# Optimization experiments

Hardware: AMD Instinct MI355X
Metric: run time of the kernel (lower is better)

## Reference

```python
import jax, jax.numpy as jnp
import numpy as np

M1 = M2 = 16      # spectral modes
CM1 = CM2 = 4     # cft modes = modes // 4
L_SEG = 4
M_CHEB = 8
PAD = 9


def _cft2d(x):
    # x: [B,C,H,W]; H,W divisible by L_SEG, segment length divisible by M_CHEB
    B, C, H, W = x.shape
    hs, ws = H // L_SEG, W // L_SEG
    seg = x.reshape(B, C, L_SEG, hs, L_SEG, ws).transpose(0, 1, 2, 4, 3, 5)
    seg = seg.reshape(B, C, L_SEG * L_SEG, hs * ws)  # row-major segment order (i,j)
    seg = seg / jnp.maximum(jnp.linalg.norm(seg, axis=-1, keepdims=True), 1e-12)
    # torch x[:,:,k::M].mean over k=0..M-1 == reshape (n//M, M), mean over rows
    coeffs = seg.reshape(B, C, L_SEG * L_SEG, (hs * ws) // M_CHEB, M_CHEB).mean(axis=3)
    coeffs = coeffs.reshape(B, C, -1)[:, :, : CM1 * CM2]
    return coeffs.reshape(B, C, CM1, CM2)  # real part; imag part is zero


def _spectral_rc(x, w1, w2, g1w, g1b, g2w, g2b):
    B, C, H, W = x.shape
    xft = jnp.fft.rfft2(x, axes=(-2, -1))
    top = jnp.einsum('bixy,ioxy->boxy', xft[:, :, :M1, :M2], w1)
    bot = jnp.einsum('bixy,ioxy->boxy', xft[:, :, H - M1:, :M2], w2)
    out_ft = jnp.zeros((B, w1.shape[1], H, W // 2 + 1), dtype=xft.dtype)
    out_ft = out_ft.at[:, :, :M1, :M2].set(top)
    out_ft = out_ft.at[:, :, H - M1:, :M2].set(bot)
    x_fno = jnp.fft.irfft2(out_ft, s=(H, W), axes=(-2, -1))
    cr = _cft2d(x)
    # torch.view_as_real interleaves (real, imag) on last axis; imag == 0
    cflat = jnp.stack([cr, jnp.zeros_like(cr)], axis=-1).reshape(B, -1)
    h = jax.nn.gelu(cflat @ g1w.T + g1b, approximate=False)
    corr = h @ g2w.T + g2b  # [B, C_out]
    return x_fno + corr[:, :, None, None]


def _forward(x, sw1r, sw1i, sw2r, sw2i, g1w, g1b, g2w, g2b, cw, cb,
             fc0w, fc0b, fc1w, fc1b, fc2w, fc2b):
    B, S1, S2, _ = x.shape
    gx = jnp.broadcast_to(jnp.linspace(0., 1., S1, dtype=x.dtype)[None, :, None, None], (B, S1, S2, 1))
    gy = jnp.broadcast_to(jnp.linspace(0., 1., S2, dtype=x.dtype)[None, None, :, None], (B, S1, S2, 1))
    h = jnp.concatenate([x, gx, gy], axis=-1) @ fc0w.T + fc0b
    h = h.transpose(0, 3, 1, 2)
    h = jnp.pad(h, ((0, 0), (0, 0), (0, PAD), (0, PAD)))
    for l in range(4):
        w1 = sw1r[l] + 1j * sw1i[l]
        w2 = sw2r[l] + 1j * sw2i[l]
        h1 = _spectral_rc(h, w1, w2, g1w[l], g1b[l], g2w[l], g2b[l])
        h2 = jnp.einsum('bchw,oc->bohw', h, cw[l]) + cb[l][None, :, None, None]
        h = h1 + h2
        if l < 3:
            h = jax.nn.gelu(h, approximate=False)
    h = h[..., :-PAD, :-PAD].transpose(0, 2, 3, 1)
    h = jax.nn.gelu(h @ fc1w.T + fc1b, approximate=False)
    return h @ fc2w.T + fc2b


def setup_inputs():
    key = jax.random.key(0)
    ks = jax.random.split(key, 20)
    B, S, Cin, Cout, Wd = 8, 119, 3, 1, 64
    f32 = jnp.float32
    scale = 1.0 / (Wd * Wd)
    return {
        'x': jax.random.normal(ks[0], (B, S, S, Cin), f32),
        'sw1r': scale * jax.random.uniform(ks[1], (4, Wd, Wd, M1, M2), f32),
        'sw1i': scale * jax.random.uniform(ks[2], (4, Wd, Wd, M1, M2), f32),
        'sw2r': scale * jax.random.uniform(ks[3], (4, Wd, Wd, M1, M2), f32),
        'sw2i': scale * jax.random.uniform(ks[4], (4, Wd, Wd, M1, M2), f32),
        'g1w': 0.02 * jax.random.normal(ks[5], (4, 256, 2048), f32),
        'g1b': 0.02 * jax.random.normal(ks[6], (4, 256), f32),
        'g2w': 0.02 * jax.random.normal(ks[7], (4, Wd, 256), f32),
        'g2b': 0.02 * jax.random.normal(ks[8], (4, Wd), f32),
        'cw': (1.0 / 8.0) * jax.random.normal(ks[9], (4, Wd, Wd), f32),
        'cb': 0.1 * jax.random.normal(ks[10], (4, Wd), f32),
        'fc0w': 0.4 * jax.random.normal(ks[11], (Wd, Cin + 2), f32),
        'fc0b': 0.1 * jax.random.normal(ks[12], (Wd,), f32),
        'fc1w': (1.0 / 8.0) * jax.random.normal(ks[13], (128, Wd), f32),
        'fc1b': 0.1 * jax.random.normal(ks[14], (128,), f32),
        'fc2w': (1.0 / 11.3) * jax.random.normal(ks[15], (Cout, 128), f32),
        'fc2b': 0.1 * jax.random.normal(ks[16], (Cout,), f32),
    }


def reference(x, sw1r, sw1i, sw2r, sw2i, g1w, g1b, g2w, g2b, cw, cb,
              fc0w, fc0b, fc1w, fc1b, fc2w, fc2b):
    return _forward(x, sw1r, sw1i, sw2r, sw2i, g1w, g1b, g2w, g2b, cw, cb,
                    fc0w, fc0b, fc1w, fc1b, fc2w, fc2b)
```

## Files before the change

### kernel.cpp

```cpp
#include <hip/hip_runtime.h>
#include <math.h>

#define NB 8
#define NC 64
#define NH 128
#define NW 128
#define NS 119
#define NPIX 113288

typedef __attribute__((ext_vector_type(8))) short bf16x8;
typedef __attribute__((ext_vector_type(4))) float f32x4;
typedef __attribute__((ext_vector_type(4))) unsigned short ushort4v;

__device__ __forceinline__ float gelu_f(float v) {
    return 0.5f * v * (1.0f + erff(v * 0.70710678118654752f));
}

__device__ __forceinline__ unsigned short f2bf(float x) {
    unsigned int u = __builtin_bit_cast(unsigned int, x);
    u += 0x7FFFu + ((u >> 16) & 1u);
    return (unsigned short)(u >> 16);
}

__global__ void __launch_bounds__(128) k_trig(float2* __restrict__ trig) {
    int t = threadIdx.x;
    double a = (double)t * (3.14159265358979323846 / 64.0);
    trig[t] = make_float2((float)cos(a), (float)sin(a));
}

__global__ void __launch_bounds__(256) k_tabm(short* __restrict__ wmf) {
    int idx = blockIdx.x * 256 + threadIdx.x;
    int f = idx >> 9;
    int l = (idx >> 3) & 63;
    int e = idx & 7;
    int ni = f >> 2, k = f & 3;
    int w = k * 32 + (l >> 4) * 8 + e;
    int n = ni * 16 + (l & 15);
    int q = n >> 1;
    int prod = (q * w) & 127;
    double a = (double)prod * (3.14159265358979323846 / 64.0);
    float v = (float)((n & 1) ? -sin(a) : cos(a));
    wmf[idx] = (short)f2bf(v);
}

__global__ void __launch_bounds__(256) k_tc(const float* __restrict__ fc1w,
                                            const float* __restrict__ cw,
                                            float* __restrict__ fc1wT,
                                            float* __restrict__ cwT) {
    int u = blockIdx.x * 256 + threadIdx.x;
    if (u < 8192) {
        int c = u >> 7, j = u & 127;
        fc1wT[u] = fc1w[j * 64 + c];
    } else {
        int v = u - 8192;
        int l = v >> 12, idx = v & 4095;
        int c = idx >> 6, o = idx & 63;
        cwT[v] = cw[l * 4096 + o * 64 + c];
    }
}

__global__ void __launch_bounds__(256) k_fc0(const float* __restrict__ x,
                                             const float* __restrict__ w,
                                             const float* __restrict__ bia,
                                             float* __restrict__ h) {
    __shared__ float sw[320];
    __shared__ float sb[64];
    int t = threadIdx.x;
    for (int u = t; u < 320; u += 256) sw[u] = w[u];
    if (t < 64) sb[t] = bia[t];
    __syncthreads();
    int p = blockIdx.x * 256 + t;
    int b = p >> 14;
    int rem = p & 16383;
    int r = rem >> 7, wc = rem & 127;
    float v0 = 0.f, v1 = 0.f, v2 = 0.f, gx = 0.f, gy = 0.f;
    bool inside = (r < NS) && (wc < NS);
    if (inside) {
        const float* xp = x + ((size_t)(b * NS + r) * NS + wc) * 3;
        v0 = xp[0]; v1 = xp[1]; v2 = xp[2];
        gx = (float)r * (1.0f / 118.0f);
        gy = (float)wc * (1.0f / 118.0f);
    }
    float* hp = h + (size_t)b * NC * NH * NW + rem;
    for (int c = 0; c < 64; ++c) {
        float val = 0.f;
        if (inside) {
            const float* wr = sw + c * 5;
            val = v0 * wr[0] + v1 * wr[1] + v2 * wr[2] + gx * wr[3] + gy * wr[4] + sb[c];
        }
        hp[c * (NH * NW)] = val;
    }
}

__global__ void __launch_bounds__(256) k_dft2(const float* __restrict__ h,
                                              float2* __restrict__ xft,
                                              float* __restrict__ cr,
                                              const short* __restrict__ wmf,
                                              const float2* __restrict__ trig) {
    __shared__ __align__(16) short sxb[32][136];
    __shared__ float2 sT[128][17];
    __shared__ float2 st[128];
    __shared__ float s_cs[2][32][8];
    __shared__ float s_cq[2][32][8];
    int t = threadIdx.x;
    int bc = blockIdx.x;
    if (t < 128) st[t] = trig[t];
    int lane = t & 63, wv = t >> 6;
    int mi = wv >> 1, ni = wv & 1;
    bf16x8 bfrag[4];
    {
        const short* wp = wmf + ((size_t)(ni * 4) * 64 + lane) * 8;
#pragma unroll
        for (int k = 0; k < 4; ++k) bfrag[k] = *(const bf16x8*)(wp + k * 512);
    }
    const float* src = h + (size_t)bc * 16384;
    const short* abase = &sxb[mi * 16 + (lane & 15)][(lane >> 4) * 8];
    for (int it = 0; it < 4; ++it) {
        __syncthreads();
#pragma unroll
        for (int j = 0; j < 4; ++j) {
            int idx4 = t + j * 256;
            float4 v = *(const float4*)(src + (size_t)it * 4096 + (size_t)idx4 * 4);
            ushort4v pk;
            pk.x = f2bf(v.x); pk.y = f2bf(v.y); pk.z = f2bf(v.z); pk.w = f2bf(v.w);
            int row = idx4 >> 5, c4 = (idx4 & 31) * 4;
            *(ushort4v*)(&sxb[row][c4]) = pk;
        }
        if (it == 0) {
            int rr = t >> 3, k = t & 7;
            const float* rowp = src + rr * 128;
            float cs0 = 0.f, cq0 = 0.f, cs1 = 0.f, cq1 = 0.f;
#pragma unroll
            for (int g = 0; g < 4; ++g) {
                float a = rowp[g * 8 + k];       cs0 += a;  cq0 += a * a;
                float b = rowp[32 + g * 8 + k];  cs1 += b;  cq1 += b * b;
            }
            s_cs[0][rr][k] = cs0; s_cs[1][rr][k] = cs1;
            s_cq[0][rr][k] = cq0; s_cq[1][rr][k] = cq1;
        }
        __syncthreads();
        f32x4 D = {0.f, 0.f, 0.f, 0.f};
#pragma unroll
        for (int k = 0; k < 4; ++k) {
            bf16x8 a = *(const bf16x8*)(abase + k * 32);
            D = __builtin_amdgcn_mfma_f32_16x16x32_bf16(a, bfrag[k], D, 0, 0, 0);
        }
        int row = it * 32 + mi * 16 + ((lane >> 4) << 2);
        int col = ni * 16 + (lane & 15);
        float* sTf = (float*)&sT[0][0];
#pragma unroll
        for (int r = 0; r < 4; ++r) sTf[(size_t)(row + r) * 34 + col] = D[r];
    }
    __syncthreads();
    int ky = t & 15;
    int mlo = t >> 4;
    int kxa = mlo, kxb = 112 + mlo;
    float2 sva = st[kxa]; float sca = sva.x, ssa = -sva.y;
    float2 svb = st[kxb]; float scb = svb.x, ssb = -svb.y;
    float rea = 0.f, ima = 0.f, reb = 0.f, imb = 0.f;
    for (int h0 = 0; h0 < 128; h0 += 16) {
        float2 bva = st[(kxa * h0) & 127]; float cca = bva.x, csa = -bva.y;
        float2 bvb = st[(kxb * h0) & 127]; float ccb = bvb.x, csb = -bvb.y;
#pragma unroll
        for (int j = 0; j < 16; ++j) {
            float2 Tv = sT[h0 + j][ky];
            rea += Tv.x * cca - Tv.y * csa;
            ima += Tv.x * csa + Tv.y * cca;
            reb += Tv.x * ccb - Tv.y * csb;
            imb += Tv.x * csb + Tv.y * ccb;
            float na = cca * sca - csa * ssa; csa = cca * ssa + csa * sca; cca = na;
            float nb = ccb * scb - csb * ssb; csb = ccb * ssb + csb * scb; ccb = nb;
        }
    }
    float2* xp = xft + (size_t)bc * 512;
    xp[mlo * 16 + ky] = make_float2(rea, ima);
    xp[(mlo + 16) * 16 + ky] = make_float2(reb, imb);
    if (t < 16) {
        int half = t >> 3, k = t & 7;
        float s = 0.f, q = 0.f;
        for (int rr = 0; rr < 32; ++rr) {
            s += s_cs[half][rr][k];
#pragma unroll
            for (int kk = 0; kk < 8; ++kk) q += s_cq[half][rr][kk];
        }
        float norm = fmaxf(sqrtf(q), 1e-12f);
        cr[bc * 16 + t] = s / (128.0f * norm);
    }
}

__global__ void __launch_bounds__(512) k_mixmlp(const float2* __restrict__ xft,
                                                const float* __restrict__ w1r,
                                                const float* __restrict__ w1i,
                                                const float* __restrict__ w2r,
                                                const float* __restrict__ w2i,
                                                const float* __restrict__ cr,
                                                const float* __restrict__ g1w,
                                                const float* __restrict__ g1b,
                                                float* __restrict__ hmid,
                                                float2* __restrict__ F) {
    __shared__ __align__(16) char smem[36864];
    int t = threadIdx.x;
    int bid = blockIdx.x;
    if (bid < 512) {
        float2* s_w = (float2*)smem;
        float2* s_x = (float2*)(smem + 32768);
        int m = (bid & 7) + 8 * ((bid >> 3) & 3);
        int e = bid >> 5;
        const float* wr; const float* wi; int mm;
        if (m < 16) { wr = w1r; wi = w1i; mm = m; } else { wr = w2r; wi = w2i; mm = m - 16; }
        int off = mm * 16 + e;
        for (int u = t; u < 4096; u += 512) {
            s_w[u] = make_float2(wr[(u << 8) + off], wi[(u << 8) + off]);
        }
        {
            int bb = t >> 6, i = t & 63;
            s_x[bb * 64 + i] = xft[((size_t)(bb * 64 + i) * 32 + m) * 16 + e];
        }
        __syncthreads();
        int bb = t >> 6, o = t & 63;
        float re = 0.f, im = 0.f;
#pragma unroll 8
        for (int i = 0; i < 64; ++i) {
            float2 xv = s_x[bb * 64 + i];
            float2 wv = s_w[i * 64 + o];
            re += xv.x * wv.x - xv.y * wv.y;
            im += xv.x * wv.y + xv.y * wv.x;
        }
        F[((size_t)(bb * 16 + e) * 32 + m) * 64 + o] = make_float2(re, im);
    } else {
        float* s_cr   = (float*)smem;
        float* s_wave = (float*)(smem + 32768);
        int j = bid - 512;
        for (int u = t; u < 8192; u += 512) s_cr[u] = cr[u];
        const float* wrow = g1w + (size_t)j * 2048;
        float w0 = wrow[4 * t], w1 = wrow[4 * t + 2];
        __syncthreads();
        float acc[8];
#pragma unroll
        for (int b = 0; b < 8; ++b) {
            float2 v = *(const float2*)(s_cr + b * 1024 + 2 * t);
            acc[b] = v.x * w0 + v.y * w1;
        }
#pragma unroll
        for (int d = 32; d > 0; d >>= 1) {
#pragma unroll
            for (int b = 0; b < 8; ++b) acc[b] += __shfl_down(acc[b], d, 64);
        }
        int wv = t >> 6;
        if ((t & 63) == 0) {
#pragma unroll
            for (int b = 0; b < 8; ++b) s_wave[wv * 8 + b] = acc[b];
        }
        __syncthreads();
        if (t < 8) {
            float a = g1b[j];
            for (int q = 0; q < 8; ++q) a += s_wave[q * 8 + t];
            hmid[t * 256 + j] = gelu_f(a);
        }
    }
}

__global__ void __launch_bounds__(256, 4) k_invb(const float2* __restrict__ F,
                                                 const float* __restrict__ hin,
                                                 const float* __restrict__ cwTl,
                                                 const float* __restrict__ cbl,
                                                 const float* __restrict__ hmid,
                                                 const float* __restrict__ g2w,
                                                 const float* __restrict__ g2b,
                                                 const float2* __restrict__ trig,
                                                 float* __restrict__ hout,
                                                 int do_gelu) {
    int blk = blockIdx.x;
    int b = blk >> 7, h = blk & 127;
    __shared__ __align__(16) float s_cwT[64][64];
    __shared__ __align__(16) float2 s_g[16][64];
    __shared__ float2 s_t[128];
    __shared__ float s_co[64];
    __shared__ float s_part[4][64];
    int t = threadIdx.x;
    if (t < 128) s_t[t] = trig[t];
    {
        float* cw0 = &s_cwT[0][0];
        for (int u = t; u < 4096; u += 256) cw0[u] = cwTl[u];
    }
    {
        int o = t & 63, q = t >> 6;
        const float* hv = hmid + b * 256 + q * 64;
        const float* gw = g2w + o * 256 + q * 64;
        float a = 0.f;
#pragma unroll 8
        for (int v = 0; v < 64; ++v) a += hv[v] * gw[v];
        s_part[q][o] = a;
    }
    {
        int o = t & 63, ky0 = t >> 6;
        const float2* Fb = F + (size_t)b * 32768 + o;
        float a0r=0.f,a0i=0.f,a1r=0.f,a1i=0.f,a2r=0.f,a2i=0.f,a3r=0.f,a3i=0.f;
#pragma unroll 4
        for (int m = 0; m < 32; ++m) {
            int kx = (m < 16) ? m : (96 + m);
            float2 wz = trig[(kx * h) & 127];
            const float2* fm = Fb + m * 64;
            float2 f0 = fm[(ky0     ) * 2048];
            float2 f1 = fm[(ky0 +  4) * 2048];
            float2 f2 = fm[(ky0 +  8) * 2048];
            float2 f3 = fm[(ky0 + 12) * 2048];
            a0r += f0.x*wz.x - f0.y*wz.y; a0i += f0.x*wz.y + f0.y*wz.x;
            a1r += f1.x*wz.x - f1.y*wz.y; a1i += f1.x*wz.y + f1.y*wz.x;
            a2r += f2.x*wz.x - f2.y*wz.y; a2i += f2.x*wz.y + f2.y*wz.x;
            a3r += f3.x*wz.x - f3.y*wz.y; a3i += f3.x*wz.y + f3.y*wz.x;
        }
        s_g[ky0     ][o] = make_float2(a0r, a0i);
        s_g[ky0 +  4][o] = make_float2(a1r, a1i);
        s_g[ky0 +  8][o] = make_float2(a2r, a2i);
        s_g[ky0 + 12][o] = make_float2(a3r, a3i);
    }
    __syncthreads();
    if (t < 64)
        s_co[t] = s_part[0][t] + s_part[1][t] + s_part[2][t] + s_part[3][t]
                + g2b[t] + cbl[t];
    int ot2 = t >> 6;
    int wt6 = t & 63;
    int o0 = ot2 * 16;
    float acc[16][2];
#pragma unroll
    for (int i = 0; i < 16; ++i) { acc[i][0] = 0.f; acc[i][1] = 0.f; }
    float2 rw0 = s_t[wt6];
    float2 rw1 = s_t[wt6 + 64];
    float z0r = 1.f, z0i = 0.f, z1r = 1.f, z1i = 0.f;
    const float invn = 1.0f / 16384.0f;
    for (int ky = 0; ky < 16; ++ky) {
        float fs = (ky == 0) ? invn : (2.f * invn);
        float tc0 = fs * z0r, ts0 = fs * z0i;
        float tc1 = fs * z1r, ts1 = fs * z1i;
        const float4* gk = (const float4*)(&s_g[ky][o0]);
#pragma unroll
        for (int i2 = 0; i2 < 8; ++i2) {
            float4 g2 = gk[i2];
            acc[2*i2][0]   += g2.x * tc0 - g2.y * ts0;
            acc[2*i2][1]   += g2.x * tc1 - g2.y * ts1;
            acc[2*i2+1][0] += g2.z * tc0 - g2.w * ts0;
            acc[2*i2+1][1] += g2.z * tc1 - g2.w * ts1;
        }
        float nz0 = z0r * rw0.x - z0i * rw0.y; z0i = z0r * rw0.y + z0i * rw0.x; z0r = nz0;
        float nz1 = z1r * rw1.x - z1i * rw1.y; z1i = z1r * rw1.y + z1i * rw1.x; z1r = nz1;
    }
    const float* hp = hin + ((size_t)(b * 64) * 128 + h) * 128;
    for (int cc = 0; cc < 64; cc += 4) {
        float hv0[4], hv1[4];
#pragma unroll
        for (int c = 0; c < 4; ++c) {
            hv0[c] = hp[(size_t)(cc + c) * 16384 + wt6];
            hv1[c] = hp[(size_t)(cc + c) * 16384 + wt6 + 64];
        }
#pragma unroll
        for (int c = 0; c < 4; ++c) {
            const float4* cwp = (const float4*)(&s_cwT[cc + c][o0]);
#pragma unroll
            for (int i4 = 0; i4 < 4; ++i4) {
                float4 cv = cwp[i4];
                acc[4*i4][0]   += cv.x * hv0[c]; acc[4*i4][1]   += cv.x * hv1[c];
                acc[4*i4+1][0] += cv.y * hv0[c]; acc[4*i4+1][1] += cv.y * hv1[c];
                acc[4*i4+2][0] += cv.z * hv0[c]; acc[4*i4+2][1] += cv.z * hv1[c];
                acc[4*i4+3][0] += cv.w * hv0[c]; acc[4*i4+3][1] += cv.w * hv1[c];
            }
        }
    }
    __syncthreads();
#pragma unroll
    for (int i = 0; i < 16; ++i) {
        int o = o0 + i;
        float co = s_co[o];
        float* outp = hout + ((size_t)(b * 64 + o) * 128 + h) * 128;
        float v0 = acc[i][0] + co;
        float v1 = acc[i][1] + co;
        if (do_gelu) { v0 = gelu_f(v0); v1 = gelu_f(v1); }
        outp[wt6] = v0;
        outp[wt6 + 64] = v1;
    }
}

__global__ void __launch_bounds__(256, 2) k_invbh(const float2* __restrict__ F,
                                                  const float* __restrict__ hin,
                                                  const float* __restrict__ cwTl,
                                                  const float* __restrict__ cbl,
                                                  const float* __restrict__ hmid,
                                                  const float* __restrict__ g2w,
                                                  const float* __restrict__ g2b,
                                                  const float2* __restrict__ trig,
                                                  const float* __restrict__ fc1wT,
                                                  const float* __restrict__ fc1b,
                                                  const float* __restrict__ fc2w,
                                                  const float* __restrict__ fc2b,
                                                  float* __restrict__ out) {
    int blk = blockIdx.x;
    int b = blk / 119;
    int h = blk - b * 119;
    __shared__ __align__(16) char smem[32768];
    float*  s_cwT = (float*)smem;
    float2* s_g   = (float2*)(smem + 16384);
    float*  s_hall= (float*)smem;
    __shared__ __align__(16) float s_w8[16][128];
    __shared__ float2 s_t[128];
    __shared__ float s_co[64];
    __shared__ float s_b1[128];
    __shared__ float s_w2[128];
    __shared__ float s_red[4][132];
    __shared__ float s_part[4][64];
    int t = threadIdx.x;
    if (t < 128) s_t[t] = trig[t];
    else { s_b1[t - 128] = fc1b[t - 128]; s_w2[t - 128] = fc2w[t - 128]; }
    for (int u = t; u < 4096; u += 256) s_cwT[u] = cwTl[u];
    {
        int o = t & 63, q = t >> 6;
        const float* hv = hmid + b * 256 + q * 64;
        const float* gw = g2w + o * 256 + q * 64;
        float a = 0.f;
#pragma unroll 8
        for (int v = 0; v < 64; ++v) a += hv[v] * gw[v];
        s_part[q][o] = a;
    }
    {
        int o = t & 63, ky0 = t >> 6;
        const float2* Fb = F + (size_t)b * 32768 + o;
        float a0r=0.f,a0i=0.f,a1r=0.f,a1i=0.f,a2r=0.f,a2i=0.f,a3r=0.f,a3i=0.f;
#pragma unroll 4
        for (int m = 0; m < 32; ++m) {
            int kx = (m < 16) ? m : (96 + m);
            float2 wz = trig[(kx * h) & 127];
            const float2* fm = Fb + m * 64;
            float2 f0 = fm[(ky0     ) * 2048];
            float2 f1 = fm[(ky0 +  4) * 2048];
            float2 f2 = fm[(ky0 +  8) * 2048];
            float2 f3 = fm[(ky0 + 12) * 2048];
            a0r += f0.x*wz.x - f0.y*wz.y; a0i += f0.x*wz.y + f0.y*wz.x;
            a1r += f1.x*wz.x - f1.y*wz.y; a1i += f1.x*wz.y + f1.y*wz.x;
            a2r += f2.x*wz.x - f2.y*wz.y; a2i += f2.x*wz.y + f2.y*wz.x;
            a3r += f3.x*wz.x - f3.y*wz.y; a3i += f3.x*wz.y + f3.y*wz.x;
        }
        float2* sg = (float2*)(smem + 16384);
        sg[(ky0     ) * 64 + o] = make_float2(a0r, a0i);
        sg[(ky0 +  4) * 64 + o] = make_float2(a1r, a1i);
        sg[(ky0 +  8) * 64 + o] = make_float2(a2r, a2i);
        sg[(ky0 + 12) * 64 + o] = make_float2(a3r, a3i);
    }
    __syncthreads();
    if (t < 64)
        s_co[t] = s_part[0][t] + s_part[1][t] + s_part[2][t] + s_part[3][t]
                + g2b[t] + cbl[t];
    int ot2 = t >> 6;
    int wt6 = t & 63;
    int o0 = ot2 * 16;
    float acc[16][2];
#pragma unroll
    for (int i = 0; i < 16; ++i) { acc[i][0] = 0.f; acc[i][1] = 0.f; }
    float2 rw0 = s_t[wt6];
    float2 rw1 = s_t[wt6 + 64];
    float z0r = 1.f, z0i = 0.f, z1r = 1.f, z1i = 0.f;
    const float invn = 1.0f / 16384.0f;
    for (int ky = 0; ky < 16; ++ky) {
        float fs = (ky == 0) ? invn : (2.f * invn);
        float tc0 = fs * z0r, ts0 = fs * z0i;
        float tc1 = fs * z1r, ts1 = fs * z1i;
        const float4* gk = (const float4*)(s_g + ky * 64 + o0);
#pragma unroll
        for (int i2 = 0; i2 < 8; ++i2) {
            float4 g2 = gk[i2];
            acc[2*i2][0]   += g2.x * tc0 - g2.y * ts0;
            acc[2*i2][1]   += g2.x * tc1 - g2.y * ts1;
            acc[2*i2+1][0] += g2.z * tc0 - g2.w * ts0;
            acc[2*i2+1][1] += g2.z * tc1 - g2.w * ts1;
        }
        float nz0 = z0r * rw0.x - z0i * rw0.y; z0i = z0r * rw0.y + z0i * rw0.x; z0r = nz0;
        float nz1 = z1r * rw1.x - z1i * rw1.y; z1i = z1r * rw1.y + z1i * rw1.x; z1r = nz1;
    }
    const float* hp = hin + ((size_t)(b * 64) * 128 + h) * 128;
    for (int cc = 0; cc < 64; cc += 8) {
        float hv0[8], hv1[8];
#pragma unroll
        for (int c = 0; c < 8; ++c) {
            hv0[c] = hp[(size_t)(cc + c) * 16384 + wt6];
            hv1[c] = hp[(size_t)(cc + c) * 16384 + wt6 + 64];
        }
#pragma unroll
        for (int c = 0; c < 8; ++c) {
            const float4* cwp = (const float4*)(s_cwT + (cc + c) * 64 + o0);
#pragma unroll
            for (int i4 = 0; i4 < 4; ++i4) {
                float4 cv = cwp[i4];
                acc[4*i4][0]   += cv.x * hv0[c]; acc[4*i4][1]   += cv.x * hv1[c];
                acc[4*i4+1][0] += cv.y * hv0[c]; acc[4*i4+1][1] += cv.y * hv1[c];
                acc[4*i4+2][0] += cv.z * hv0[c]; acc[4*i4+2][1] += cv.z * hv1[c];
                acc[4*i4+3][0] += cv.w * hv0[c]; acc[4*i4+3][1] += cv.w * hv1[c];
            }
        }
    }
    __syncthreads();
#pragma unroll
    for (int i = 0; i < 16; ++i) {
        float co = s_co[o0 + i];
        s_hall[(o0 + i) * 128 + wt6]      = acc[i][0] + co;
        s_hall[(o0 + i) * 128 + wt6 + 64] = acc[i][1] + co;
    }
    int j0 = ot2 * 32;
    float a32[32][2];
#pragma unroll
    for (int i = 0; i < 32; ++i) { a32[i][0] = 0.f; a32[i][1] = 0.f; }
    for (int cc = 0; cc < 64; cc += 16) {
        __syncthreads();
        for (int u = t; u < 2048; u += 256)
            s_w8[u >> 7][u & 127] = fc1wT[(cc + (u >> 7)) * 128 + (u & 127)];
        __syncthreads();
        for (int c = 0; c < 16; ++c) {
            float hv0 = s_hall[(cc + c) * 128 + wt6];
            float hv1 = s_hall[(cc + c) * 128 + wt6 + 64];
            const float4* wp = (const float4*)(&s_w8[c][j0]);
#pragma unroll
            for (int q = 0; q < 8; ++q) {
                float4 wx = wp[q];
                a32[4*q][0]   += wx.x * hv0; a32[4*q][1]   += wx.x * hv1;
                a32[4*q+1][0] += wx.y * hv0; a32[4*q+1][1] += wx.y * hv1;
                a32[4*q+2][0] += wx.z * hv0; a32[4*q+2][1] += wx.z * hv1;
                a32[4*q+3][0] += wx.w * hv0; a32[4*q+3][1] += wx.w * hv1;
            }
        }
    }
    float sum0 = 0.f, sum1 = 0.f;
#pragma unroll
    for (int i = 0; i < 32; ++i) {
        float b1 = s_b1[j0 + i];
        float w2 = s_w2[j0 + i];
        sum0 += gelu_f(a32[i][0] + b1) * w2;
        sum1 += gelu_f(a32[i][1] + b1) * w2;
    }
    s_red[ot2][wt6] = sum0;
    s_red[ot2][wt6 + 64] = sum1;
    __syncthreads();
    if (t < NS) {
        out[b * (NS * NS) + h * NS + t] =
            fc2b[0] + s_red[0][t] + s_red[1][t] + s_red[2][t] + s_red[3][t];
    }
}

extern "C" void kernel_launch(void* const* d_in, const int* in_sizes, int n_in,
                              void* d_out, int out_size, void* d_ws, size_t ws_size,
                              hipStream_t stream) {
    const float* x    = (const float*)d_in[0];
    const float* sw1r = (const float*)d_in[1];
    const float* sw1i = (const float*)d_in[2];
    const float* sw2r = (const float*)d_in[3];
    const float* sw2i = (const float*)d_in[4];
    const float* g1w  = (const float*)d_in[5];
    const float* g1b  = (const float*)d_in[6];
    const float* g2w  = (const float*)d_in[7];
    const float* g2b  = (const float*)d_in[8];
    const float* cw   = (const float*)d_in[9];
    const float* cb   = (const float*)d_in[10];
    const float* fc0w = (const float*)d_in[11];
    const float* fc0b = (const float*)d_in[12];
    const float* fc1w = (const float*)d_in[13];
    const float* fc1b = (const float*)d_in[14];
    const float* fc2w = (const float*)d_in[15];
    const float* fc2b = (const float*)d_in[16];
    float* out = (float*)d_out;

    char* ws = (char*)d_ws;
    const size_t SZ_H   = (size_t)NB * NC * NH * NW * 4;
    const size_t SZ_XFT = (size_t)NB * NC * 32 * 16 * 8;
    const size_t SZ_F   = SZ_XFT;
    size_t off = 0;
    float2* trig = (float2*)(ws + off); off += 1024;
    short*  wmf  = (short*)(ws + off);  off += 4096 * 2;
    float*  f1T  = (float*)(ws + off);  off += 8192 * 4;
    float*  cwT  = (float*)(ws + off);  off += 16384 * 4;
    off = (off + 255) & ~(size_t)255;
    float*  hA   = (float*)(ws + off);  off += SZ_H;
    float*  hB   = (float*)(ws + off);  off += SZ_H;
    float2* xft  = (float2*)(ws + off); off += SZ_XFT;
    float2* F    = (float2*)(ws + off); off += SZ_F;
    float*  cr   = (float*)(ws + off);  off += (size_t)NB * NC * 16 * 4;
    float*  hmid = (float*)(ws + off);  off += (size_t)NB * 256 * 4;
    (void)ws_size; (void)in_sizes; (void)n_in; (void)out_size;

    k_trig<<<1, 128, 0, stream>>>(trig);
    k_tabm<<<16, 256, 0, stream>>>(wmf);
    k_tc<<<96, 256, 0, stream>>>(fc1w, cw, f1T, cwT);
    k_fc0<<<512, 256, 0, stream>>>(x, fc0w, fc0b, hA);

    float* hcur = hA;
    float* hnxt = hB;
    for (int l = 0; l < 4; ++l) {
        const float* w1r = sw1r + (size_t)l * 1048576;
        const float* w1i = sw1i + (size_t)l * 1048576;
        const float* w2r = sw2r + (size_t)l * 1048576;
        const float* w2i = sw2i + (size_t)l * 1048576;
        const float* g1w_l = g1w + (size_t)l * 524288;
        const float* g1b_l = g1b + l * 256;
        const float* g2w_l = g2w + (size_t)l * 16384;
        const float* g2b_l = g2b + l * 64;
        const float* cwT_l = cwT + (size_t)l * 4096;
        const float* cb_l  = cb + l * 64;

        k_dft2<<<512, 256, 0, stream>>>(hcur, xft, cr, wmf, trig);
        k_mixmlp<<<768, 512, 0, stream>>>(xft, w1r, w1i, w2r, w2i,
                                          cr, g1w_l, g1b_l, hmid, F);
        if (l < 3) {
            k_invb<<<1024, 256, 0, stream>>>(F, hcur, cwT_l, cb_l, hmid,
                                             g2w_l, g2b_l, trig, hnxt, 1);
            float* tmp = hcur; hcur = hnxt; hnxt = tmp;
        } else {
            k_invbh<<<NB * NS, 256, 0, stream>>>(F, hcur, cwT_l, cb_l, hmid,
                                                 g2w_l, g2b_l, trig,
                                                 f1T, fc1b, fc2w, fc2b, out);
        }
    }
}
```

Before: 453.4 us.

## Use split-bf16 MFMA for inverse DFT and 1x1 conv in k_invb

Replaces the scalar FP32 inverse-DFT-along-W and channel-mixing accumulation in k_invb with bf16 MFMA 16x16x32 instructions. A 3-way split (hi/lo bf16 pairs, four products) approximates FP32 accuracy. A new precomputed twiddle table with the scale factors baked in supplies the B operand. The hin row is staged in LDS as transposed hi/lo bf16, and cw is read directly into registers. This trades the large scalar FMA count for matrix-core work, at the cost of conversion overhead, more LDS and lower occupancy (launch bound 3).

```diff
diff --git a/kernel.cpp b/kernel.cpp
--- a/kernel.cpp
+++ b/kernel.cpp
@@ -20,6 +20,10 @@
     unsigned int u = __builtin_bit_cast(unsigned int, x);
     u += 0x7FFFu + ((u >> 16) & 1u);
     return (unsigned short)(u >> 16);
+}
+__device__ __forceinline__ float bf2f(unsigned short s) {
+    unsigned int u = (unsigned int)s << 16;
+    return __builtin_bit_cast(float, u);
 }
 
 __global__ void __launch_bounds__(128) k_trig(float2* __restrict__ trig) {
@@ -41,6 +45,21 @@
     double a = (double)prod * (3.14159265358979323846 / 64.0);
     float v = (float)((n & 1) ? -sin(a) : cos(a));
     wmf[idx] = (short)f2bf(v);
+}
+
+__global__ void __launch_bounds__(256) k_tabi(short* __restrict__ bt) {
+    int idx = blockIdx.x * 256 + threadIdx.x;
+    int wt = idx >> 9, l = (idx >> 3) & 63, e = idx & 7;
+    int k = (l >> 4) * 8 + e;
+    int w = wt * 16 + (l & 15);
+    int q = k >> 1;
+    double a = (double)((q * w) & 127) * (3.14159265358979323846 / 64.0);
+    double fs = (q == 0) ? (1.0 / 16384.0) : (2.0 / 16384.0);
+    float val = (float)((k & 1) ? (-fs * sin(a)) : (fs * cos(a)));
+    unsigned short hi = f2bf(val);
+    unsigned short lo = f2bf(val - bf2f(hi));
+    bt[idx] = (short)hi;
+    bt[4096 + idx] = (short)lo;
 }
 
 __global__ void __launch_bounds__(256) k_tc(const float* __restrict__ fc1w,
@@ -260,7 +279,7 @@
     }
 }
 
-__global__ void __launch_bounds__(256, 4) k_invb(const float2* __restrict__ F,
+__global__ void __launch_bounds__(256, 3) k_invb(const float2* __restrict__ F,
                                                  const float* __restrict__ hin,
                                                  const float* __restrict__ cwTl,
                                                  const float* __restrict__ cbl,
@@ -268,21 +287,17 @@
                                                  const float* __restrict__ g2w,
                                                  const float* __restrict__ g2b,
                                                  const float2* __restrict__ trig,
+                                                 const short* __restrict__ bt,
                                                  float* __restrict__ hout,
                                                  int do_gelu) {
     int blk = blockIdx.x;
     int b = blk >> 7, h = blk & 127;
-    __shared__ __align__(16) float s_cwT[64][64];
-    __shared__ __align__(16) float2 s_g[16][64];
-    __shared__ float2 s_t[128];
+    __shared__ __align__(16) short s_ht[2][128][72];
+    __shared__ __align__(16) short s_ab[2 * 4 * 64 * 8];
     __shared__ float s_co[64];
     __shared__ float s_part[4][64];
     int t = threadIdx.x;
-    if (t < 128) s_t[t] = trig[t];
-    {
-        float* cw0 = &s_cwT[0][0];
-        for (int u = t; u < 4096; u += 256) cw0[u] = cwTl[u];
-    }
+    int lane = t & 63, wv = t >> 6;
     {
         int o = t & 63, q = t >> 6;
         const float* hv = hmid + b * 256 + q * 64;
@@ -295,88 +310,95 @@
     {
         int o = t & 63, ky0 = t >> 6;
         const float2* Fb = F + (size_t)b * 32768 + o;
-        float a0r=0.f,a0i=0.f,a1r=0.f,a1i=0.f,a2r=0.f,a2i=0.f,a3r=0.f,a3i=0.f;
+        float ar[4] = {0.f, 0.f, 0.f, 0.f};
+        float ai[4] = {0.f, 0.f, 0.f, 0.f};
 #pragma unroll 4
         for (int m = 0; m < 32; ++m) {
             int kx = (m < 16) ? m : (96 + m);
             float2 wz = trig[(kx * h) & 127];
             const float2* fm = Fb + m * 64;
-            float2 f0 = fm[(ky0     ) * 2048];
-            float2 f1 = fm[(ky0 +  4) * 2048];
-            float2 f2 = fm[(ky0 +  8) * 2048];
-            float2 f3 = fm[(ky0 + 12) * 2048];
-            a0r += f0.x*wz.x - f0.y*wz.y; a0i += f0.x*wz.y + f0.y*wz.x;
-            a1r += f1.x*wz.x - f1.y*wz.y; a1i += f1.x*wz.y + f1.y*wz.x;
-            a2r += f2.x*wz.x - f2.y*wz.y; a2i += f2.x*wz.y + f2.y*wz.x;
-            a3r += f3.x*wz.x - f3.y*wz.y; a3i += f3.x*wz.y + f3.y*wz.x;
-        }
-        s_g[ky0     ][o] = make_float2(a0r, a0i);
-        s_g[ky0 +  4][o] = make_float2(a1r, a1i);
-        s_g[ky0 +  8][o] = make_float2(a2r, a2i);
-        s_g[ky0 + 12][o] = make_float2(a3r, a3i);
+#pragma unroll
+            for (int j = 0; j < 4; ++j) {
+                float2 f = fm[(ky0 + 4 * j) * 2048];
+                ar[j] += f.x * wz.x - f.y * wz.y;
+                ai[j] += f.x * wz.y + f.y * wz.x;
+            }
+        }
+        int otile = o >> 4, ol = o & 15;
+#pragma unroll
+        for (int j = 0; j < 4; ++j) {
+            unsigned short hr = f2bf(ar[j]);
+            unsigned short hii = f2bf(ai[j]);
+            unsigned short lr = f2bf(ar[j] - bf2f(hr));
+            unsigned short li = f2bf(ai[j] - bf2f(hii));
+            int lanei = (j << 4) | ol;
+            *(unsigned int*)(s_ab + (otile * 64 + lanei) * 8 + 2 * ky0)
+                = (unsigned int)hr | ((unsigned int)hii << 16);
+            *(unsigned int*)(s_ab + ((4 + otile) * 64 + lanei) * 8 + 2 * ky0)
+                = (unsigned int)lr | ((unsigned int)li << 16);
+        }
+    }
+    {
+        const float* hp = hin + (size_t)(b * 64) * 16384 + h * 128;
+        for (int u = t; u < 8192; u += 256) {
+            int c = u >> 7, w = u & 127;
+            float x = hp[(size_t)c * 16384 + w];
+            unsigned short hi = f2bf(x);
+            s_ht[0][w][c] = (short)hi;
+            s_ht[1][w][c] = (short)f2bf(x - bf2f(hi));
+        }
     }
     __syncthreads();
     if (t < 64)
         s_co[t] = s_part[0][t] + s_part[1][t] + s_part[2][t] + s_part[3][t]
                 + g2b[t] + cbl[t];
-    int ot2 = t >> 6;
-    int wt6 = t & 63;
-    int o0 = ot2 * 16;
-    float acc[16][2];
-#pragma unroll
-    for (int i = 0; i < 16; ++i) { acc[i][0] = 0.f; acc[i][1] = 0.f; }
-    float2 rw0 = s_t[wt6];
-    float2 rw1 = s_t[wt6 + 64];
-    float z0r = 1.f, z0i = 0.f, z1r = 1.f, z1i = 0.f;
-    const float invn = 1.0f / 16384.0f;
-    for (int ky = 0; ky < 16; ++ky) {
-        float fs = (ky == 0) ? invn : (2.f * invn);
-        float tc0 = fs * z0r, ts0 = fs * z0i;
-        float tc1 = fs * z1r, ts1 = fs * z1i;
-        const float4* gk = (const float4*)(&s_g[ky][o0]);
-#pragma unroll
-        for (int i2 = 0; i2 < 8; ++i2) {
-            float4 g2 = gk[i2];
-            acc[2*i2][0]   += g2.x * tc0 - g2.y * ts0;
-            acc[2*i2][1]   += g2.x * tc1 - g2.y * ts1;
-            acc[2*i2+1][0] += g2.z * tc0 - g2.w * ts0;
-            acc[2*i2+1][1] += g2.z * tc1 - g2.w * ts1;
-        }
-        float nz0 = z0r * rw0.x - z0i * rw0.y; z0i = z0r * rw0.y + z0i * rw0.x; z0r = nz0;
-        float nz1 = z1r * rw1.x - z1i * rw1.y; z1i = z1r * rw1.y + z1i * rw1.x; z1r = nz1;
-    }
-    const float* hp = hin + ((size_t)(b * 64) * 128 + h) * 128;
-    for (int cc = 0; cc < 64; cc += 4) {
-        float hv0[4], hv1[4];
-#pragma unroll
-        for (int c = 0; c < 4; ++c) {
-            hv0[c] = hp[(size_t)(cc + c) * 16384 + wt6];
-            hv1[c] = hp[(size_t)(cc + c) * 16384 + wt6 + 64];
-        }
-#pragma unroll
-        for (int c = 0; c < 4; ++c) {
-            const float4* cwp = (const float4*)(&s_cwT[cc + c][o0]);
-#pragma unroll
-            for (int i4 = 0; i4 < 4; ++i4) {
-                float4 cv = cwp[i4];
-                acc[4*i4][0]   += cv.x * hv0[c]; acc[4*i4][1]   += cv.x * hv1[c];
-                acc[4*i4+1][0] += cv.y * hv0[c]; acc[4*i4+1][1] += cv.y * hv1[c];
-                acc[4*i4+2][0] += cv.z * hv0[c]; acc[4*i4+2][1] += cv.z * hv1[c];
-                acc[4*i4+3][0] += cv.w * hv0[c]; acc[4*i4+3][1] += cv.w * hv1[c];
+    bf16x8 cwa_hi[2], cwa_lo[2];
+    {
+        int orow = wv * 16 + (lane & 15);
+#pragma unroll
+        for (int kc = 0; kc < 2; ++kc) {
+#pragma unroll
+            for (int e = 0; e < 8; ++e) {
+                int c = kc * 32 + (lane >> 4) * 8 + e;
+                float x = cwTl[c * 64 + orow];
+                unsigned short hi = f2bf(x);
+                cwa_hi[kc][e] = (short)hi;
+                cwa_lo[kc][e] = (short)f2bf(x - bf2f(hi));
             }
         }
     }
+    bf16x8 ga_hi = *(const bf16x8*)(s_ab + (wv * 64 + lane) * 8);
+    bf16x8 ga_lo = *(const bf16x8*)(s_ab + ((4 + wv) * 64 + lane) * 8);
     __syncthreads();
 #pragma unroll
-    for (int i = 0; i < 16; ++i) {
-        int o = o0 + i;
-        float co = s_co[o];
-        float* outp = hout + ((size_t)(b * 64 + o) * 128 + h) * 128;
-        float v0 = acc[i][0] + co;
-        float v1 = acc[i][1] + co;
-        if (do_gelu) { v0 = gelu_f(v0); v1 = gelu_f(v1); }
-        outp[wt6] = v0;
-        outp[wt6 + 64] = v1;
+    for (int wt = 0; wt < 8; ++wt) {
+        f32x4 acc = {0.f, 0.f, 0.f, 0.f};
+        bf16x8 bh = *(const bf16x8*)(bt + (wt * 64 + lane) * 8);
+        bf16x8 bl = *(const bf16x8*)(bt + 4096 + (wt * 64 + lane) * 8);
+        acc = __builtin_amdgcn_mfma_f32_16x16x32_bf16(ga_hi, bh, acc, 0, 0, 0);
+        acc = __builtin_amdgcn_mfma_f32_16x16x32_bf16(ga_hi, bl, acc, 0, 0, 0);
+        acc = __builtin_amdgcn_mfma_f32_16x16x32_bf16(ga_lo, bh, acc, 0, 0, 0);
+        acc = __builtin_amdgcn_mfma_f32_16x16x32_bf16(ga_lo, bl, acc, 0, 0, 0);
+#pragma unroll
+        for (int kc = 0; kc < 2; ++kc) {
+            const short* hb = &s_ht[0][wt * 16 + (lane & 15)][kc * 32 + (lane >> 4) * 8];
+            const short* lb = &s_ht[1][wt * 16 + (lane & 15)][kc * 32 + (lane >> 4) * 8];
+            bf16x8 hbh = *(const bf16x8*)hb;
+            bf16x8 hbl = *(const bf16x8*)lb;
+            acc = __builtin_amdgcn_mfma_f32_16x16x32_bf16(cwa_hi[kc], hbh, acc, 0, 0, 0);
+            acc = __builtin_amdgcn_mfma_f32_16x16x32_bf16(cwa_hi[kc], hbl, acc, 0, 0, 0);
+            acc = __builtin_amdgcn_mfma_f32_16x16x32_bf16(cwa_lo[kc], hbh, acc, 0, 0, 0);
+            acc = __builtin_amdgcn_mfma_f32_16x16x32_bf16(cwa_lo[kc], hbl, acc, 0, 0, 0);
+        }
+        int wcol = wt * 16 + (lane & 15);
+        int obase = wv * 16 + ((lane >> 4) << 2);
+#pragma unroll
+        for (int r = 0; r < 4; ++r) {
+            int o = obase + r;
+            float v = acc[r] + s_co[o];
+            if (do_gelu) v = gelu_f(v);
+            hout[((size_t)(b * 64 + o) * 128 + h) * 128 + wcol] = v;
+        }
     }
 }
 
@@ -571,6 +593,7 @@
     size_t off = 0;
     float2* trig = (float2*)(ws + off); off += 1024;
     short*  wmf  = (short*)(ws + off);  off += 4096 * 2;
+    short*  bt   = (short*)(ws + off);  off += 8192 * 2;
     float*  f1T  = (float*)(ws + off);  off += 8192 * 4;
     float*  cwT  = (float*)(ws + off);  off += 16384 * 4;
     off = (off + 255) & ~(size_t)255;
@@ -584,6 +607,7 @@
 
     k_trig<<<1, 128, 0, stream>>>(trig);
     k_tabm<<<16, 256, 0, stream>>>(wmf);
+    k_tabi<<<16, 256, 0, stream>>>(bt);
     k_tc<<<96, 256, 0, stream>>>(fc1w, cw, f1T, cwT);
     k_fc0<<<512, 256, 0, stream>>>(x, fc0w, fc0b, hA);
 
@@ -606,7 +630,7 @@
                                           cr, g1w_l, g1b_l, hmid, F);
         if (l < 3) {
             k_invb<<<1024, 256, 0, stream>>>(F, hcur, cwT_l, cb_l, hmid,
-                                             g2w_l, g2b_l, trig, hnxt, 1);
+                                             g2w_l, g2b_l, trig, bt, hnxt, 1);
             float* tmp = hcur; hcur = hnxt; hnxt = tmp;
         } else {
             k_invbh<<<NB * NS, 256, 0, stream>>>(F, hcur, cwT_l, cb_l, hmid,
```

After: 437.4 us, median of 2. 3.5% less time.
